# Kernel tuning notes

Measured on AMD Instinct MI355X. Metric: run time of the kernel, lower is better.

Reference implementation:

```python
import jax, jax.numpy as jnp
import numpy as np

B, S, D = 16, 2048, 128


def setup_inputs() -> dict:
    k = jax.random.key(0)
    k1, k2, k3, k4 = jax.random.split(k, 4)
    query = jax.random.normal(k1, (B, S, D), dtype=jnp.float32)
    key = jax.random.normal(k2, (B, S, D), dtype=jnp.float32)
    value = jax.random.normal(k3, (B, S, D), dtype=jnp.float32)
    # per-query tensor-valued inverse scale; shift away from zero for stable division
    inv_scale_factor = jax.random.uniform(k4, (B, S, 1), dtype=jnp.float32) + 0.5
    dropout_p = jnp.float32(0.1)
    return {"query": query, "key": key, "value": value,
            "inv_scale_factor": inv_scale_factor, "dropout_p": dropout_p}


def reference(query, key, value, inv_scale_factor, dropout_p):
    # QK^T: [B, Sq, Sk]
    qk = jnp.einsum('bqd,bkd->bqk', query, key)
    # tensor-valued scale divide (broadcast [B, Sq, 1] over keys)
    scaled_qk = qk / inv_scale_factor
    softmax_qk = jax.nn.softmax(scaled_qk, axis=-1)
    # dropout with a fixed RNG key (deterministic reference)
    keep_prob = 1.0 - dropout_p
    mask = jax.random.bernoulli(jax.random.key(42), keep_prob, softmax_qk.shape)
    dropout_qk = jnp.where(mask, softmax_qk / keep_prob, jnp.float32(0.0))
    # AV: [B, Sq, Dv]
    return jnp.einsum('bqk,bkv->bqv', dropout_qk, value)
```

## Files before the change

kernel.cpp:

```cpp
#include <hip/hip_runtime.h>
#include <stdint.h>


#define B_ 16
#define S_ 2048
#define D_ 128
#define TQ 64
#define TK 64
#define NT (S_ / TK)
#define VSTR 72
#define PSTR 40
#define VTILE (D_ * VSTR)
#define KST_ELEMS ((size_t)B_ * S_ * D_)

typedef float f32x4 __attribute__((ext_vector_type(4)));
typedef _Float16 f16x8 __attribute__((ext_vector_type(8)));
typedef _Float16 f16x4 __attribute__((ext_vector_type(4)));

#define DPP_ROR(x, ctrl) \
  __int_as_float(__builtin_amdgcn_update_dpp(0, __float_as_int(x), (ctrl), 0xf, 0xf, true))
__device__ __forceinline__ float row16_max(float x) {
  x = fmaxf(x, DPP_ROR(x, 0x128));
  x = fmaxf(x, DPP_ROR(x, 0x124));
  x = fmaxf(x, DPP_ROR(x, 0x122));
  x = fmaxf(x, DPP_ROR(x, 0x121));
  return x;
}
__device__ __forceinline__ float row16_sum(float x) {
  x += DPP_ROR(x, 0x128);
  x += DPP_ROR(x, 0x124);
  x += DPP_ROR(x, 0x122);
  x += DPP_ROR(x, 0x121);
  return x;
}

__device__ __forceinline__ uint2 threefry2x32_0_42(uint32_t x0, uint32_t x1) {
  const uint32_t k0 = 0u, k1 = 42u;
  const uint32_t k2 = 0x1BD11BDAu ^ k0 ^ k1;
  x0 += k0; x1 += k1;
#define TFR(r) { x0 += x1; x1 = __builtin_rotateleft32(x1, r); x1 ^= x0; }
  TFR(13) TFR(15) TFR(26) TFR(6)
  x0 += k1; x1 += k2 + 1u;
  TFR(17) TFR(29) TFR(16) TFR(24)
  x0 += k2; x1 += k0 + 2u;
  TFR(13) TFR(15) TFR(26) TFR(6)
  x0 += k0; x1 += k1 + 3u;
  TFR(17) TFR(29) TFR(16) TFR(24)
  x0 += k1; x1 += k2 + 4u;
  TFR(13) TFR(15) TFR(26) TFR(6)
  x0 += k2; x1 += k0 + 5u;
#undef TFR
  return make_uint2(x0, x1);
}

__device__ __forceinline__ uint32_t jax_bits(uint32_t j) {
  const uint2 tf = threefry2x32_0_42(0u, j);
  return tf.x ^ tf.y;
}

__global__ __launch_bounds__(256)
void prep_k(const float* __restrict__ K, _Float16* __restrict__ Kst) {
  const size_t i = ((size_t)blockIdx.x * 256 + threadIdx.x) * 4;
  const float4 x = *(const float4*)(K + i);
  f16x4 h = {(_Float16)x.x, (_Float16)x.y, (_Float16)x.z, (_Float16)x.w};
  *(f16x4*)(Kst + i) = h;
}

__global__ __launch_bounds__(256)
void prep_v(const float* __restrict__ V, _Float16* __restrict__ Vst) {
  __shared__ _Float16 sT[64 * 132];
  const int b = blockIdx.y, kt = blockIdx.x, t = threadIdx.x;
  const int key = t >> 2, dq = t & 3;
  const float* vp = V + ((size_t)(b * S_ + kt * 64 + key)) * D_ + dq * 32;
  #pragma unroll
  for (int i = 0; i < 8; ++i) {
    const float4 x = *(const float4*)(vp + i * 4);
    _Float16* d = &sT[key * 132 + dq * 32 + i * 4];
    d[0] = (_Float16)x.x; d[1] = (_Float16)x.y;
    d[2] = (_Float16)x.z; d[3] = (_Float16)x.w;
  }
  __syncthreads();
  _Float16* tile = Vst + (size_t)(b * NT + kt) * VTILE;
  #pragma unroll
  for (int it = 0; it < 4; ++it) {
    const int idx = t * 4 + it;
    const int d = idx >> 3, kg = idx & 7;
    f16x8 v;
    #pragma unroll
    for (int j = 0; j < 8; ++j) v[j] = sT[(kg * 8 + j) * 132 + d];
    *(f16x8*)&tile[d * VSTR + kg * 8] = v;
  }
}

__global__ __launch_bounds__(512, 4)
void attn_mfma_kernel(const float* __restrict__ Q, const _Float16* __restrict__ Kst,
                      const _Float16* __restrict__ Vst, const float* __restrict__ ISF,
                      const float* __restrict__ DP, float* __restrict__ OUT) {
  __shared__ __align__(16) char smem[47104];
  char* const sVT0 = smem;
  char* const sVT1 = smem + 18432;
  _Float16* const sP = (_Float16*)(smem + 36864);
  float* const sO1 = (float*)smem;
  float* const sM1 = (float*)(smem + 32768);
  float* const sL1 = (float*)(smem + 33024);

  const int t    = threadIdx.x;
  const int lane = t & 63;
  const int l15  = lane & 15;
  const int quad = lane >> 4;
  const int w    = t >> 6;
  const int qsub = w >> 1;
  const int kph  = w & 1;
  const int b    = blockIdx.y;
  const int qb   = blockIdx.x * TQ + qsub * 16;

  const float kp = 1.0f - DP[0];
  const uint32_t TH9 = (__float_as_uint(1.0f + kp) & 0x7FFFFFu) << 9;

  float m_[4], l_[4];
  uint32_t jq[4];
  #pragma unroll
  for (int r = 0; r < 4; ++r) {
    m_[r] = -INFINITY;
    l_[r] = 0.0f;
    jq[r] = ((uint32_t)b << 22)
          + (uint32_t)(qb + quad * 4 + r) * (uint32_t)S_;
  }

  f16x8 qf[4];
  {
    const int qrow = qb + l15;
    const float qs = 1.4426950408889634f / ISF[b * S_ + qrow];
    const float* qp = Q + ((size_t)(b * S_ + qrow)) * D_;
    #pragma unroll
    for (int c = 0; c < 4; ++c) {
      const float4 a  = *(const float4*)(qp + c * 32 + quad * 8);
      const float4 d2 = *(const float4*)(qp + c * 32 + quad * 8 + 4);
      const float xs[8] = {a.x, a.y, a.z, a.w, d2.x, d2.y, d2.z, d2.w};
      f16x8 h;
      #pragma unroll
      for (int j = 0; j < 8; ++j) h[j] = (_Float16)(xs[j] * qs);
      qf[c] = h;
    }
  }

  f32x4 accO[8];
  #pragma unroll
  for (int i = 0; i < 8; ++i) accO[i] = (f32x4){0.f, 0.f, 0.f, 0.f};

  _Float16* const pwv = &sP[w * 16 * PSTR];

#define STAGE_V(VT, SV)                                                        \
  {                                                                            \
    const char* vsrc = (const char*)(Vst + (size_t)(b * NT + (VT)) * VTILE);   \
    for (int s8 = w; s8 < 18; s8 += 8) {                                       \
      __builtin_amdgcn_global_load_lds(                                        \
          (const unsigned int*)(vsrc + s8 * 1024 + lane * 16),                 \
          (unsigned int*)((SV) + s8 * 1024), 16, 0, 0);                        \
    }                                                                          \
  }

  STAGE_V(0, sVT0)
  __syncthreads();

  for (int kt = 0; kt < NT; ++kt) {
    const int cur = kt & 1;
    char* const sVc = cur ? sVT1 : sVT0;

    const _Float16* kb = Kst + ((size_t)(b * S_ + kt * TK + kph * 32)) * D_;
    f16x8 kf[2][4];
    #pragma unroll
    for (int n = 0; n < 2; ++n)
      #pragma unroll
      for (int c = 0; c < 4; ++c)
        kf[n][c] = *(const f16x8*)(kb + (n * 16 + l15) * D_ + c * 32 + quad * 8);

    f32x4 s[2];
    #pragma unroll
    for (int n = 0; n < 2; ++n) {
      f32x4 a0 = (f32x4){0.f, 0.f, 0.f, 0.f};
      #pragma unroll
      for (int c = 0; c < 4; ++c)
        a0 = __builtin_amdgcn_mfma_f32_16x16x32_f16(qf[c], kf[n][c], a0, 0, 0, 0);
      s[n] = a0;
    }

    if (kt + 1 < NT) {
      char* const sVn = cur ? sVT0 : sVT1;
      STAGE_V(kt + 1, sVn)
    }

    uint32_t rb[2][4];
    #pragma unroll
    for (int n = 0; n < 2; ++n) {
      const uint32_t jcol = (uint32_t)(kt * TK + kph * 32 + n * 16 + l15);
      #pragma unroll
      for (int r = 0; r < 4; ++r)
        rb[n][r] = jax_bits(jq[r] + jcol);
    }

    float mx[4];
    int changed = 0;
    #pragma unroll
    for (int r = 0; r < 4; ++r) {
      mx[r] = row16_max(fmaxf(s[0][r], s[1][r]));
      changed |= (mx[r] > m_[r] + 8.0f);
    }
    if (__ballot(changed) != 0ull) {
      #pragma unroll
      for (int r = 0; r < 4; ++r) {
        const float mnew = fmaxf(m_[r], mx[r]);
        const float alpha = __builtin_amdgcn_exp2f(m_[r] - mnew);
        m_[r] = mnew;
        l_[r] *= alpha;
        #pragma unroll
        for (int i = 0; i < 8; ++i) accO[i][r] *= alpha;
      }
    }
    #pragma unroll
    for (int r = 0; r < 4; ++r) {
      const float p0 = __builtin_amdgcn_exp2f(s[0][r] - m_[r]);
      const float p1 = __builtin_amdgcn_exp2f(s[1][r] - m_[r]);
      s[0][r] = p0;
      s[1][r] = p1;
      l_[r] += p0 + p1;
    }

    #pragma unroll
    for (int n = 0; n < 2; ++n) {
      const int col = n * 16 + l15;
      #pragma unroll
      for (int r = 0; r < 4; ++r) {
        const float pf = (rb[n][r] < TH9) ? s[n][r] : 0.0f;
        pwv[(quad * 4 + r) * PSTR + col] = (_Float16)pf;
      }
    }
    __threadfence_block();

    {
      const f16x8 ap = *(const f16x8*)&pwv[l15 * PSTR + quad * 8];
      const _Float16* vb = (const _Float16*)sVc;
      #pragma unroll
      for (int d8 = 0; d8 < 8; ++d8) {
        const f16x8 bv = *(const f16x8*)&vb[(d8 * 16 + l15) * VSTR
                                            + kph * 32 + quad * 8];
        accO[d8] = __builtin_amdgcn_mfma_f32_16x16x32_f16(ap, bv, accO[d8], 0, 0, 0);
      }
    }

    __syncthreads();
  }
#undef STAGE_V

  #pragma unroll
  for (int r = 0; r < 4; ++r)
    l_[r] = row16_sum(l_[r]);

  if (kph == 1) {
    if (l15 == 0) {
      #pragma unroll
      for (int r = 0; r < 4; ++r) {
        const int gr = qsub * 16 + quad * 4 + r;
        sM1[gr] = m_[r];
        sL1[gr] = l_[r];
      }
    }
    #pragma unroll
    for (int d8 = 0; d8 < 8; ++d8)
      #pragma unroll
      for (int r = 0; r < 4; ++r) {
        const int gr = qsub * 16 + quad * 4 + r;
        sO1[gr * D_ + d8 * 16 + l15] = accO[d8][r];
      }
  }
  __syncthreads();
  if (kph == 0) {
    float a0s[4], a1s[4];
    #pragma unroll
    for (int r = 0; r < 4; ++r) {
      const int gr = qsub * 16 + quad * 4 + r;
      const float m1  = sM1[gr];
      const float l1v = sL1[gr];
      const float mf = fmaxf(m_[r], m1);
      const float a0 = __builtin_amdgcn_exp2f(m_[r] - mf);
      const float a1 = __builtin_amdgcn_exp2f(m1 - mf);
      const float inv = 1.0f / ((a0 * l_[r] + a1 * l1v) * kp);
      a0s[r] = a0 * inv;
      a1s[r] = a1 * inv;
    }
    #pragma unroll
    for (int d8 = 0; d8 < 8; ++d8)
      #pragma unroll
      for (int r = 0; r < 4; ++r) {
        const int gr = qsub * 16 + quad * 4 + r;
        const float o1 = sO1[gr * D_ + d8 * 16 + l15];
        OUT[((size_t)(b * S_ + blockIdx.x * TQ + gr)) * D_ + d8 * 16 + l15] =
            accO[d8][r] * a0s[r] + o1 * a1s[r];
      }
  }
}

extern "C" void kernel_launch(void* const* d_in, const int* in_sizes, int n_in,
                              void* d_out, int out_size, void* d_ws, size_t ws_size,
                              hipStream_t stream) {
  const float* q   = (const float*)d_in[0];
  const float* k   = (const float*)d_in[1];
  const float* v   = (const float*)d_in[2];
  const float* isf = (const float*)d_in[3];
  const float* dp  = (const float*)d_in[4];
  float* out = (float*)d_out;

  _Float16* kst = (_Float16*)d_ws;
  _Float16* vst = kst + KST_ELEMS;

  prep_k<<<dim3(4096), dim3(256), 0, stream>>>(k, kst);
  prep_v<<<dim3(NT, B_), dim3(256), 0, stream>>>(v, vst);

  dim3 grid(S_ / TQ, B_);
  attn_mfma_kernel<<<grid, dim3(512), 0, stream>>>(q, kst, vst, isf, dp, out);
}
```

Baseline: 333.0 us.

## Load V fragments directly from global memory, drop LDS staging, merge prep kernels

The attention kernel no longer double-buffers transposed V tiles in LDS through global_load_lds plus a per-iteration __syncthreads. Each wave now reads its V MFMA operands straight from global (L2-resident) memory into registers, and the per-tile barrier is removed. The V tile stride changes from padded 72 to 64, and the K and V fp16 conversion kernels are fused into one launch. This removes barrier stalls and the launch gap but raises register pressure, so launch bounds drop to 3 waves per SIMD. The P write/read through LDS now relies only on __threadfence_block, with no barrier inside the loop.

```diff
diff --git a/kernel.cpp b/kernel.cpp
--- a/kernel.cpp
+++ b/kernel.cpp
@@ -8,9 +8,8 @@
 #define TQ 64
 #define TK 64
 #define NT (S_ / TK)
-#define VSTR 72
 #define PSTR 40
-#define VTILE (D_ * VSTR)
+#define VTILE (64 * D_)
 #define KST_ELEMS ((size_t)B_ * S_ * D_)
 
 typedef float f32x4 __attribute__((ext_vector_type(4)));
@@ -59,17 +58,19 @@
 }
 
 __global__ __launch_bounds__(256)
-void prep_k(const float* __restrict__ K, _Float16* __restrict__ Kst) {
-  const size_t i = ((size_t)blockIdx.x * 256 + threadIdx.x) * 4;
-  const float4 x = *(const float4*)(K + i);
-  f16x4 h = {(_Float16)x.x, (_Float16)x.y, (_Float16)x.z, (_Float16)x.w};
-  *(f16x4*)(Kst + i) = h;
-}
-
-__global__ __launch_bounds__(256)
-void prep_v(const float* __restrict__ V, _Float16* __restrict__ Vst) {
+void prep_kv(const float* __restrict__ K, const float* __restrict__ V,
+             _Float16* __restrict__ Kst, _Float16* __restrict__ Vst) {
   __shared__ _Float16 sT[64 * 132];
-  const int b = blockIdx.y, kt = blockIdx.x, t = threadIdx.x;
+  const int t = threadIdx.x;
+  if (blockIdx.x < 4096) {
+    const size_t i = ((size_t)blockIdx.x * 256 + t) * 4;
+    const float4 x = *(const float4*)(K + i);
+    f16x4 h = {(_Float16)x.x, (_Float16)x.y, (_Float16)x.z, (_Float16)x.w};
+    *(f16x4*)(Kst + i) = h;
+    return;
+  }
+  const int idx = blockIdx.x - 4096;
+  const int b = idx >> 5, kt = idx & 31;
   const int key = t >> 2, dq = t & 3;
   const float* vp = V + ((size_t)(b * S_ + kt * 64 + key)) * D_ + dq * 32;
   #pragma unroll
@@ -83,23 +84,21 @@
   _Float16* tile = Vst + (size_t)(b * NT + kt) * VTILE;
   #pragma unroll
   for (int it = 0; it < 4; ++it) {
-    const int idx = t * 4 + it;
-    const int d = idx >> 3, kg = idx & 7;
+    const int i2 = t * 4 + it;
+    const int d = i2 >> 3, kg = i2 & 7;
     f16x8 v;
     #pragma unroll
     for (int j = 0; j < 8; ++j) v[j] = sT[(kg * 8 + j) * 132 + d];
-    *(f16x8*)&tile[d * VSTR + kg * 8] = v;
-  }
-}
-
-__global__ __launch_bounds__(512, 4)
+    *(f16x8*)&tile[d * 64 + kg * 8] = v;
+  }
+}
+
+__global__ __launch_bounds__(512, 3)
 void attn_mfma_kernel(const float* __restrict__ Q, const _Float16* __restrict__ Kst,
                       const _Float16* __restrict__ Vst, const float* __restrict__ ISF,
                       const float* __restrict__ DP, float* __restrict__ OUT) {
-  __shared__ __align__(16) char smem[47104];
-  char* const sVT0 = smem;
-  char* const sVT1 = smem + 18432;
-  _Float16* const sP = (_Float16*)(smem + 36864);
+  __shared__ __align__(16) char smem[33280];
+  _Float16* const sP = (_Float16*)smem;
   float* const sO1 = (float*)smem;
   float* const sM1 = (float*)(smem + 32768);
   float* const sL1 = (float*)(smem + 33024);
@@ -150,23 +149,7 @@
 
   _Float16* const pwv = &sP[w * 16 * PSTR];
 
-#define STAGE_V(VT, SV)                                                        \
-  {                                                                            \
-    const char* vsrc = (const char*)(Vst + (size_t)(b * NT + (VT)) * VTILE);   \
-    for (int s8 = w; s8 < 18; s8 += 8) {                                       \
-      __builtin_amdgcn_global_load_lds(                                        \
-          (const unsigned int*)(vsrc + s8 * 1024 + lane * 16),                 \
-          (unsigned int*)((SV) + s8 * 1024), 16, 0, 0);                        \
-    }                                                                          \
-  }
-
-  STAGE_V(0, sVT0)
-  __syncthreads();
-
   for (int kt = 0; kt < NT; ++kt) {
-    const int cur = kt & 1;
-    char* const sVc = cur ? sVT1 : sVT0;
-
     const _Float16* kb = Kst + ((size_t)(b * S_ + kt * TK + kph * 32)) * D_;
     f16x8 kf[2][4];
     #pragma unroll
@@ -174,6 +157,21 @@
       #pragma unroll
       for (int c = 0; c < 4; ++c)
         kf[n][c] = *(const f16x8*)(kb + (n * 16 + l15) * D_ + c * 32 + quad * 8);
+
+    const _Float16* vb = Vst + (size_t)(b * NT + kt) * VTILE + kph * 32;
+    f16x8 vf[8];
+    #pragma unroll
+    for (int d8 = 0; d8 < 8; ++d8)
+      vf[d8] = *(const f16x8*)&vb[(d8 * 16 + l15) * 64 + quad * 8];
+
+    uint32_t rb[2][4];
+    #pragma unroll
+    for (int n = 0; n < 2; ++n) {
+      const uint32_t jcol = (uint32_t)(kt * TK + kph * 32 + n * 16 + l15);
+      #pragma unroll
+      for (int r = 0; r < 4; ++r)
+        rb[n][r] = jax_bits(jq[r] + jcol);
+    }
 
     f32x4 s[2];
     #pragma unroll
@@ -183,20 +181,6 @@
       for (int c = 0; c < 4; ++c)
         a0 = __builtin_amdgcn_mfma_f32_16x16x32_f16(qf[c], kf[n][c], a0, 0, 0, 0);
       s[n] = a0;
-    }
-
-    if (kt + 1 < NT) {
-      char* const sVn = cur ? sVT0 : sVT1;
-      STAGE_V(kt + 1, sVn)
-    }
-
-    uint32_t rb[2][4];
-    #pragma unroll
-    for (int n = 0; n < 2; ++n) {
-      const uint32_t jcol = (uint32_t)(kt * TK + kph * 32 + n * 16 + l15);
-      #pragma unroll
-      for (int r = 0; r < 4; ++r)
-        rb[n][r] = jax_bits(jq[r] + jcol);
     }
 
     float mx[4];
@@ -239,23 +223,17 @@
 
     {
       const f16x8 ap = *(const f16x8*)&pwv[l15 * PSTR + quad * 8];
-      const _Float16* vb = (const _Float16*)sVc;
-      #pragma unroll
-      for (int d8 = 0; d8 < 8; ++d8) {
-        const f16x8 bv = *(const f16x8*)&vb[(d8 * 16 + l15) * VSTR
-                                            + kph * 32 + quad * 8];
-        accO[d8] = __builtin_amdgcn_mfma_f32_16x16x32_f16(ap, bv, accO[d8], 0, 0, 0);
-      }
-    }
-
-    __syncthreads();
-  }
-#undef STAGE_V
+      #pragma unroll
+      for (int d8 = 0; d8 < 8; ++d8)
+        accO[d8] = __builtin_amdgcn_mfma_f32_16x16x32_f16(ap, vf[d8], accO[d8], 0, 0, 0);
+    }
+  }
 
   #pragma unroll
   for (int r = 0; r < 4; ++r)
     l_[r] = row16_sum(l_[r]);
 
+  __syncthreads();
   if (kph == 1) {
     if (l15 == 0) {
       #pragma unroll
@@ -313,8 +291,7 @@
   _Float16* kst = (_Float16*)d_ws;
   _Float16* vst = kst + KST_ELEMS;
 
-  prep_k<<<dim3(4096), dim3(256), 0, stream>>>(k, kst);
-  prep_v<<<dim3(NT, B_), dim3(256), 0, stream>>>(v, vst);
+  prep_kv<<<dim3(4096 + 512), dim3(256), 0, stream>>>(k, v, kst, vst);
 
   dim3 grid(S_ / TQ, B_);
   attn_mfma_kernel<<<grid, dim3(512), 0, stream>>>(q, kst, vst, isf, dp, out);
```

After: 342.4 us. 1.03x slower.
